# Optimization experiments

Hardware: AMD Instinct MI355X
Metric: run time of the kernel (lower is better)

The kernel has to match this reference:

```python
import jax, jax.numpy as jnp
import numpy as np

B = 1024
NIF = 2048   # n_image_features
V = 10000    # vocab_size
E = 512      # embedding_dim
H = 1024     # hidden_size
L = 32       # max_sentence_length
ND = 3       # num distractors


def _lstm_cell(x, h, c, Wih, Whh, bih, bhh):
    # torch LSTMCell: gates ordered i, f, g, o
    g = x @ Wih.T + bih + h @ Whh.T + bhh
    i, f, gc, o = jnp.split(g, 4, axis=-1)
    c = jax.nn.sigmoid(f) * c + jax.nn.sigmoid(i) * jnp.tanh(gc)
    h = jax.nn.sigmoid(o) * jnp.tanh(c)
    return h, c


def setup_inputs() -> dict:
    key = jax.random.key(0)
    ks = jax.random.split(key, 20)
    s = 0.02
    inp = {
        "target": jax.random.normal(ks[0], (B, NIF), jnp.float32),
        "distractors": jax.random.normal(ks[1], (ND, B, NIF), jnp.float32),
        "start_token_idx": 1,
        "max_sentence_length": L,
        # Sender params
        "W_aff": s * jax.random.normal(ks[2], (H, NIF), jnp.float32),
        "b_aff": jnp.zeros((H,), jnp.float32),
        "emb_s": s * jax.random.normal(ks[3], (V, E), jnp.float32),
        "Wih_s": s * jax.random.normal(ks[4], (4 * H, E), jnp.float32),
        "Whh_s": s * jax.random.normal(ks[5], (4 * H, H), jnp.float32),
        "bih_s": jnp.zeros((4 * H,), jnp.float32),
        "bhh_s": jnp.zeros((4 * H,), jnp.float32),
        "Wp": s * jax.random.normal(ks[6], (V, H), jnp.float32),
        "bp": jnp.zeros((V,), jnp.float32),
        # Receiver params
        "emb_r": s * jax.random.normal(ks[7], (V, E), jnp.float32),
        "Wih_r": s * jax.random.normal(ks[8], (4 * H, E), jnp.float32),
        "Whh_r": s * jax.random.normal(ks[9], (4 * H, H), jnp.float32),
        "bih_r": jnp.zeros((4 * H,), jnp.float32),
        "bhh_r": jnp.zeros((4 * H,), jnp.float32),
        "W_out": s * jax.random.normal(ks[10], (NIF, H), jnp.float32),
        "b_out": jnp.zeros((NIF,), jnp.float32),
    }
    return inp


def reference(target, distractors, start_token_idx, max_sentence_length,
              W_aff, b_aff, emb_s, Wih_s, Whh_s, bih_s, bhh_s, Wp, bp,
              emb_r, Wih_r, Whh_r, bih_r, bhh_r, W_out, b_out):
    Bt = target.shape[0]

    # ---- Sender: greedy decode (eval-mode argmax, matching greedy=True) ----
    h0 = target @ W_aff.T + b_aff
    c0 = jnp.zeros_like(h0)
    w0 = emb_s[jnp.full((Bt,), start_token_idx, dtype=jnp.int32)]

    def send_step(carry, _):
        h, c, w = carry
        h, c = _lstm_cell(w, h, c, Wih_s, Whh_s, bih_s, bhh_s)
        logits = h @ Wp.T + bp                         # [B, V]
        idx = jnp.argmax(logits, axis=-1)              # greedy token
        logp = jnp.take_along_axis(jax.nn.log_softmax(logits, axis=-1),
                                   idx[:, None], axis=-1)[:, 0]
        w = emb_s[idx]
        return (h, c, w), (idx, logp)

    _, (message, logps) = jax.lax.scan(send_step, (h0, c0, w0), None,
                                       length=max_sentence_length)
    message = message.T            # [B, L]
    log_prob = logps[-1]           # log_prob of last sampled word, [B]

    # ---- Receiver: encode message ----
    hr = jnp.zeros((Bt, H), jnp.float32)
    cr = jnp.zeros((Bt, H), jnp.float32)

    def recv_step(carry, w_idx):
        h, c = carry
        h, c = _lstm_cell(emb_r[w_idx], h, c, Wih_r, Whh_r, bih_r, bhh_r)
        return (h, c), None

    (hr, cr), _ = jax.lax.scan(recv_step, (hr, cr), message.T)
    r = hr @ W_out.T + b_out       # [B, NIF]

    # ---- Hinge loss over distractors ----
    r_T = r.T                                       # [NIF, B]
    t_r = target @ r_T                              # [B, B]
    d_r = jnp.einsum('nbf,fc->nbc', distractors, r_T)  # [ND, B, B]
    loss = jnp.sum(jnp.maximum(0.0, 1.0 - t_r[None] + d_r), axis=0)  # [B, B]
    loss = -loss * log_prob        # broadcast [B] over last dim, as in torch
    return jnp.mean(loss)
```

## Files before the change

### kernel.cpp

```cpp
#include <hip/hip_runtime.h>
#include <hip/hip_bf16.h>
#include <cstdint>
#include <cstddef>

#define Bc   1024
#define NIFc 2048
#define Vc   10000
#define Ec   512
#define Hc   1024
#define Lc   32
#define NDc  3
#define G4c  4096
#define NTv  79
#define TMLD 80
#define XLD  3584
#define XOFF 512
#define RLD  1536

typedef __attribute__((ext_vector_type(4))) float f32x4;
typedef __attribute__((ext_vector_type(8))) short s16x8;
typedef __attribute__((ext_vector_type(4))) short s16x4;

__device__ __host__ __forceinline__ int rperm_orig(int p) {
    return ((p >> 4) & 3) * Hc + (p >> 6) * 16 + (p & 15);
// ... 207 lines not shown

    for (int kt = 0; kt < Hc / GBK; ++kt) {
        __syncthreads();
        #pragma unroll
        for (int r = 0; r < 4; ++r) {
            int ldsbase = (r * 256 + wave * 64) * 8;
            gld_lds16(As + ldsbase, ag[r]);
            gld_lds16(Ws + ldsbase, wg[r]);
            ag[r] += GBK;
            wg[r] += GBK;
        }
        __syncthreads();
        #pragma unroll
        for (int c = 0; c < 2; ++c) {
            s16x8 af[4], wf[4];
            int q = c * 4 + quad;
            #pragma unroll
            for (int i = 0; i < 4; ++i) {
                int m = hm + i * 16 + lm;
                af[i] = *(const s16x8*)(As + ((m << 3) + (q ^ (m & 7))) * 8);
                int n = hn + i * 16 + lm;
                wf[i] = *(const s16x8*)(Ws + ((n << 3) + (q ^ (n & 7))) * 8);
            }
            #pragma unroll
            for (int i = 0; i < 4; ++i)
                #pragma unroll
                for (int j = 0; j < 4; ++j)
                    acc[i][j] = __builtin_amdgcn_mfma_f32_16x16x32_bf16(
                        af[i], wf[j], acc[i][j], 0, 0, 0);
        }
    }

    const int u = ((n0 + hn) >> 6) * 16 + lm;
    int pc[4];
    float bv[4];
    #pragma unroll
    for (int g = 0; g < 4; ++g) {
        pc[g] = n0 + hn + g * 16 + lm;
        bv[g] = biasp[pc[g]];
    }
    #pragma unroll
    for (int i = 0; i < 4; ++i) {
        #pragma unroll
        for (int rr = 0; rr < 4; ++rr) {
            int b = m0 + hm + i * 16 + quad * 4 + rr;
            const __hip_bfloat16* xr = Xg + (size_t)tok[b] * G4c;
            float gi = acc[i][0][rr] + bv[0] + __bfloat162float(xr[pc[0]]);
            float gf = acc[i][1][rr] + bv[1] + __bfloat162float(xr[pc[1]]);
            float gg = acc[i][2][rr] + bv[2] + __bfloat162float(xr[pc[2]]);
            float go = acc[i][3][rr] + bv[3] + __bfloat162float(xr[pc[3]]);
            float si = 1.0f / (1.0f + expf(-gi));
            float sf = 1.0f / (1.0f + expf(-gf));
            float so = 1.0f / (1.0f + expf(-go));
            size_t cix = (size_t)b * Hc + u;
            float cc = sf * cr[cix] + si * tanhf(gg);
            cr[cix] = cc;
            xh_out[(size_t)b * RLD + Ec + u] = __float2bfloat16(so * tanhf(cc));
        }
    }
}

__global__ __launch_bounds__(256) void gemm_recv_final(
    const __hip_bfloat16* __restrict__ A, const __hip_bfloat16* __restrict__ W,
    const float* __restrict__ biasp, const __hip_bfloat16* __restrict__ Xg,
    const int* __restrict__ tok, float* __restrict__ cr,
    __hip_bfloat16* __restrict__ xh_out)
{
    __shared__ GemmSmem sm;
    recv_gemm_cell_body(sm, A, W, biasp, Xg, tok, cr, xh_out,
                        blockIdx.x & 31, blockIdx.x >> 5);
}

__global__ __launch_bounds__(256) void gemm_bf16_tn(
    const __hip_bfloat16* __restrict__ A, int lda,
    const __hip_bfloat16* __restrict__ W, int ldw,
    const float* __restrict__ bias, float* __restrict__ C,
    int M, int N, int K, float* __restrict__ tile_max, int tmld)
{
    __shared__ GemmSmem sm;
    gemm_body<0>(sm, A, lda, W, ldw, bias, C, M, N, K, blockIdx.x, blockIdx.y,
                 tile_max, tmld);
}

__global__ __launch_bounds__(256) void gemm_bf16_obf(
    const __hip_bfloat16* __restrict__ A, int lda,
    const __hip_bfloat16* __restrict__ W, int ldw,
    __hip_bfloat16* __restrict__ C, int M, int N, int K)
{
    __shared__ GemmSmem sm;
    gemm_body<1>(sm, A, lda, W, ldw, nullptr, C, M, N, K, blockIdx.x,
                 blockIdx.y, nullptr, 0);
}

__global__ __launch_bounds__(256) void gemm_bf16_sk2(
    const __hip_bfloat16* __restrict__ A, int lda,
    const __hip_bfloat16* __restrict__ W, int ldw,
    float* __restrict__ Cpart, int M, int N, int Ksub)
{
    __shared__ GemmSmem sm;
    int z = blockIdx.z;
    gemm_body<0>(sm, A + (size_t)z * Ksub, lda, W + (size_t)z * Ksub, ldw,
                 nullptr, Cpart + (size_t)z * M * N, M, N, Ksub, blockIdx.x,
                 blockIdx.y, nullptr, 0);
}

template<int LOGBF>
__global__ __launch_bounds__(256) void gemm_fused_step(
    int nb_g,
    const __hip_bfloat16* __restrict__ Ag, const __hip_bfloat16* __restrict__ Wg,
    float* __restrict__ Cg,
    const __hip_bfloat16* __restrict__ Al, const __hip_bfloat16* __restrict__ Wl,
    const float* __restrict__ bl, void* __restrict__ Cl,
    float* __restrict__ tmax,
    const __hip_bfloat16* __restrict__ Ar, const __hip_bfloat16* __restrict__ Wr,
    const float* __restrict__ biasrp, const __hip_bfloat16* __restrict__ Xgr,
    const int* __restrict__ tokr, float* __restrict__ cr,
    __hip_bfloat16* __restrict__ xh_out)
{
    __shared__ GemmSmem sm;
    int bid = blockIdx.x;
    if (bid < nb_g) {
        gemm_body<0>(sm, Ag, XLD, Wg, XLD, nullptr, Cg,
                     Bc, G4c, 3072, bid & 31, bid >> 5, nullptr, 0);
    } else if (bid < nb_g + 632) {
        int rem = bid - nb_g;
        int by = rem / NTv, bx = rem - by * NTv;
        gemm_body<LOGBF>(sm, Al, XLD, Wl, Hc, bl, Cl, Bc, Vc, Hc, bx, by,
                         tmax, TMLD);
    } else {
        int rem = bid - nb_g - 632;
        recv_gemm_cell_body(sm, Ar, Wr, biasrp, Xgr, tokr, cr, xh_out,
                            rem & 31, rem >> 5);
    }
}

__global__ __launch_bounds__(256) void split3_a_kernel(
    const float* __restrict__ in, int ldin,
    __hip_bfloat16* __restrict__ out, int ldo, int coff, int M, int K)
{
    int i = blockIdx.x * 256 + threadIdx.x;
    if (i >= M * K) return;
    int m = i / K, k = i - m * K;
    float v = in[(size_t)m * ldin + k];
    __hip_bfloat16 hi = __float2bfloat16(v);
    float lo = v - __bfloat162float(hi);
    __hip_bfloat16* row = out + (size_t)m * ldo + coff;
    row[k] = hi;
    row[K + k] = __float2bfloat16(lo);
    row[2 * K + k] = hi;
}

__global__ __launch_bounds__(256) void split3_w_kernel(
    const float* __restrict__ in, int ldin,
    __hip_bfloat16* __restrict__ out, int ldo, int coff, int M, int K)
{
    int i = blockIdx.x * 256 + threadIdx.x;
    if (i >= M * K) return;
    int m = i / K, k = i - m * K;
    float v = in[(size_t)m * ldin + k];
    __hip_bfloat16 hi = __float2bfloat16(v);
    float lo = v - __bfloat162float(hi);
    __hip_bfloat16* row = out + (size_t)m * ldo + coff;
    row[k] = hi;
    row[K + k] = hi;
    row[2 * K + k] = __float2bfloat16(lo);
}

__global__ __launch_bounds__(256) void cast2d_kernel(
    const float* __restrict__ in, int ldin,
    __hip_bfloat16* __restrict__ out, int ldo, int coff, int M, int K)
{
    int i = blockIdx.x * 256 + threadIdx.x;
    if (i >= M * K) return;
    int m = i / K, k = i - m * K;
    out[(size_t)m * ldo + coff + k] = __float2bfloat16(in[(size_t)m * ldin + k]);
}

__global__ __launch_bounds__(256) void cast2d_perm_kernel(
    const float* __restrict__ in, int ldin,
    __hip_bfloat16* __restrict__ out, int ldo, int coff, int M, int K)
{
    int i = blockIdx.x * 256 + threadIdx.x;
    if (i >= M * K) return;
    int p = i / K, k = i - p * K;
    out[(size_t)p * ldo + coff + k] =
        __float2bfloat16(in[(size_t)rperm_orig(p) * ldin + k]);
}

__global__ __launch_bounds__(256) void gather_cast_kernel(
    const float* __restrict__ emb, int E, const int* __restrict__ idx,
    int stride, __hip_bfloat16* __restrict__ out, int ldo, int coff, int Brows)
{
    int i = blockIdx.x * 256 + threadIdx.x;
    if (i >= Brows * E) return;
    int b = i / E, k = i - b * E;
    out[(size_t)b * ldo + coff + k] =
        __float2bfloat16(emb[(size_t)idx[(size_t)b * stride] * E + k]);
}

__global__ __launch_bounds__(256) void add_vec_kernel(
    const float* __restrict__ a, const float* __restrict__ b,
    float* __restrict__ o, int n)
{
    int i = blockIdx.x * 256 + threadIdx.x;
    if (i < n) o[i] = a[i] + b[i];
}

__global__ __launch_bounds__(256) void add_vec_perm_kernel(
    const float* __restrict__ a, const float* __restrict__ b,
    float* __restrict__ o, int n)
{
    int i = blockIdx.x * 256 + threadIdx.x;
    if (i < n) { int s = rperm_orig(i); o[i] = a[s] + b[s]; }
}

__device__ __forceinline__ short bf16bits(float x) {
    __hip_bfloat16 t = __float2bfloat16(x);
    return *reinterpret_cast<short*>(&t);
}

__device__ __forceinline__ float b16f(short s) {
    return __bfloat162float(*reinterpret_cast<__hip_bfloat16*>(&s));
}

__global__ __launch_bounds__(256) void lstm_fused_s(
    const float* __restrict__ gp0, const float* __restrict__ gp1,
    const float* __restrict__ bias, float* __restrict__ h,
    float* __restrict__ c, __hip_bfloat16* __restrict__ h3x,
    const __hip_bfloat16* __restrict__ xg, const int* __restrict__ tok,
    int tstride)
{
    int i = blockIdx.x * 256 + threadIdx.x;
    if (i >= Bc * Hc / 4) return;
    int b = i >> 8;
    int j = (i & 255) * 4;
    size_t g0 = (size_t)b * G4c + j;
    f32x4 gi = *(const f32x4*)(gp0 + g0) + *(const f32x4*)(gp1 + g0)
             + *(const f32x4*)(bias + j);
    f32x4 gf = *(const f32x4*)(gp0 + g0 + Hc) + *(const f32x4*)(gp1 + g0 + Hc)
             + *(const f32x4*)(bias + Hc + j);
    f32x4 gg = *(const f32x4*)(gp0 + g0 + 2 * Hc) + *(const f32x4*)(gp1 + g0 + 2 * Hc)
             + *(const f32x4*)(bias + 2 * Hc + j);
    f32x4 go = *(const f32x4*)(gp0 + g0 + 3 * Hc) + *(const f32x4*)(gp1 + g0 + 3 * Hc)
             + *(const f32x4*)(bias + 3 * Hc + j);
    if (xg) {
        const __hip_bfloat16* xr = xg + (size_t)tok[(size_t)b * tstride] * G4c;
        s16x4 xi = *(const s16x4*)(xr + j);
        s16x4 xf = *(const s16x4*)(xr + Hc + j);
        s16x4 xc = *(const s16x4*)(xr + 2 * Hc + j);
        s16x4 xo = *(const s16x4*)(xr + 3 * Hc + j);
        #pragma unroll
        for (int k = 0; k < 4; ++k) {
            gi[k] += b16f(xi[k]);
            gf[k] += b16f(xf[k]);
            gg[k] += b16f(xc[k]);
            go[k] += b16f(xo[k]);
        }
    }
    size_t hix = (size_t)b * Hc + j;
    f32x4 cv = *(const f32x4*)(c + hix);
    f32x4 cn, hv;
    s16x4 hi4, lo4;
    #pragma unroll
    for (int k = 0; k < 4; ++k) {
        float si = 1.0f / (1.0f + expf(-gi[k]));
        float sf = 1.0f / (1.0f + expf(-gf[k]));
        float so = 1.0f / (1.0f + expf(-go[k]));
        float cc = sf * cv[k] + si * tanhf(gg[k]);
        cn[k] = cc;
        float hh = so * tanhf(cc);
        hv[k] = hh;
        hi4[k] = bf16bits(hh);
        lo4[k] = bf16bits(hh - __bfloat162float(__float2bfloat16(hh)));
    }
    *(f32x4*)(c + hix) = cn;
    *(f32x4*)(h + hix) = hv;
    __hip_bfloat16* row = h3x + (size_t)b * XLD + XOFF;
    *(s16x4*)(row + j) = hi4;
    *(s16x4*)(row + Hc + j) = lo4;
    *(s16x4*)(row + 2 * Hc + j) = hi4;
}

__global__ __launch_bounds__(256) void combine_h0_kernel(
    const float* __restrict__ p0, const float* __restrict__ p1,
    const float* __restrict__ bias, float* __restrict__ h,
    __hip_bfloat16* __restrict__ h3x)
{
    int i = blockIdx.x * 256 + threadIdx.x;
    if (i >= Bc * Hc / 4) return;
    int b = i >> 8;
    int j = (i & 255) * 4;
    size_t ix = (size_t)b * Hc + j;
    f32x4 v = *(const f32x4*)(p0 + ix) + *(const f32x4*)(p1 + ix)
            + *(const f32x4*)(bias + j);
    *(f32x4*)(h + ix) = v;
    s16x4 hi4, lo4;
// ... 121 lines not shown
    __syncthreads();
    int nqt = nq < 32 ? nq : 32;

    for (int qi = 0; qi < nqt; qi += 2) {
        int ti = qi + (tid >> 7);
        if (ti < nqt) {
            int j = qt[ti] * 128 + (tid & 127);
            if (j < Vc) {
                float v = row[j];
                if (v >= m - delta) {
                    int k = atomicAdd(&cnt, 1);
                    if (k < 64) cand[k] = j;
                }
            }
        }
    }
    __syncthreads();
    int nc = cnt < 64 ? cnt : 64;

    const float* hrow = h + (size_t)b * Hc;
    for (int cix = wave; cix < nc; cix += 4) {
        int j = cand[cix];
        const float* wrow = Wp + (size_t)j * Hc;
        float part = 0.0f;
        #pragma unroll
        for (int kk = 0; kk < 4; ++kk) {
            int k = kk * 256 + lane * 4;
            f32x4 hv = *(const f32x4*)(hrow + k);
            f32x4 wv = *(const f32x4*)(wrow + k);
            part = fmaf(hv.x, wv.x, part);
            part = fmaf(hv.y, wv.y, part);
            part = fmaf(hv.z, wv.z, part);
            part = fmaf(hv.w, wv.w, part);
        }
        #pragma unroll
        for (int off = 1; off < 64; off <<= 1)
            part += __shfl_xor(part, off);
        if (lane == 0) score[cix] = part + bp[j];
    }
    __syncthreads();
    if (tid == 0) {
        float bv = -__builtin_inff();
        int bj = 0x7fffffff;
        for (int cix = 0; cix < nc; ++cix) {
            float v = score[cix];
            int j = cand[cix];
            if (v > bv || (v == bv && j < bj)) { bv = v; bj = j; }
        }
        sbestv = bv;
        sbestj = bj;
        msg_t[b] = bj;
    }
    __syncthreads();
    const int bestj = sbestj;

    if (want_logp) {
        float s = 0.0f;
        const f32x4* row4 = (const f32x4*)row;
        for (int j = tid; j < Vc / 4; j += 256) {
            f32x4 v = row4[j];
            s += expf(v.x - m) + expf(v.y - m) + expf(v.z - m) + expf(v.w - m);
        }
        redm[tid] = s;
        __syncthreads();
        #pragma unroll
        for (int st = 128; st > 0; st >>= 1) {
            if (tid < st) redm[tid] += redm[tid + st];
            __syncthreads();
        }
        if (tid == 0) logp[b] = sbestv - (m + logf(redm[0]));
    }

    if (xdst && tid < 128) {
        int k = tid * 4;
        f32x4 e = *(const f32x4*)(emb + (size_t)bestj * Ec + k);
        s16x4 h4;
        #pragma unroll
        for (int kk = 0; kk < 4; ++kk) h4[kk] = bf16bits(e[kk]);
        *(s16x4*)(xdst + (size_t)b * XLD + k) = h4;
    }
}

template<int LGBF>
__global__ __launch_bounds__(256) void argmax_lstm_step(
    const void* __restrict__ logits_v, const float* __restrict__ tmax,
    const float* __restrict__ h, const float* __restrict__ Wp,
    const float* __restrict__ bp, int* __restrict__ msg_t,
    float* __restrict__ logp, int want_logp,
    int do_s, const float* __restrict__ gp0,
    const float* __restrict__ bias_s, float* __restrict__ h_s,
    float* __restrict__ c_s, __hip_bfloat16* __restrict__ h3x,
    const __hip_bfloat16* __restrict__ Xg_s)
{
    const int b = blockIdx.x;
    const int tid = threadIdx.x;
    const int lane = tid & 63;
    const int wave = tid >> 6;
    const __hip_bfloat16* rowb = (const __hip_bfloat16*)logits_v + (size_t)b * Vc;
    const float* rowf = (const float*)logits_v + (size_t)b * Vc;

    __shared__ float stm[128];
    __shared__ float redm[256];
    __shared__ float reds[256];
    __shared__ int   qt[32];
    __shared__ int   nq, cnt;
    __shared__ int   cand[64];
    __shared__ float score[64];
    __shared__ float sbestv;
    __shared__ int   sbestj;

    float tv = (tid < NTv) ? tmax[(size_t)b * TMLD + tid] : -__builtin_inff();
    if (tid < 128) stm[tid] = tv;
    redm[tid] = tv;
    reds[tid] = (tid < NTv) ? tv : 0.0f;
    if (tid == 0) { nq = 0; cnt = 0; }
    __syncthreads();
    #pragma unroll
    for (int s = 128; s > 0; s >>= 1) {
        if (tid < s) {
            redm[tid] = fmaxf(redm[tid], redm[tid + s]);
            reds[tid] += reds[tid + s];
        }
        __syncthreads();
    }
    const float m = redm[0];
    const float spread = m - reds[0] * (1.0f / NTv);
    const float delta = 0.08f * spread + 1e-6f * (1.0f + fabsf(m));

    if (tid < NTv && stm[tid] >= m - delta) {
        int k = atomicAdd(&nq, 1);
        if (k < 32) qt[k] = tid;
    }
    __syncthreads();
    int nqt = nq < 32 ? nq : 32;

    for (int qi = 0; qi < nqt; qi += 2) {
        int ti = qi + (tid >> 7);
        if (ti < nqt) {
            int j = qt[ti] * 128 + (tid & 127);
            if (j < Vc) {
                float v = LGBF ? __bfloat162float(rowb[j]) : rowf[j];
                if (v >= m - delta) {
                    int k = atomicAdd(&cnt, 1);
                    if (k < 64) cand[k] = j;
                }
            }
        }
    }
    __syncthreads();
    int nc = cnt < 64 ? cnt : 64;

    const float* hrow = h + (size_t)b * Hc;
    for (int cix = wave; cix < nc; cix += 4) {
        int j = cand[cix];
        const float* wrow = Wp + (size_t)j * Hc;
        float part = 0.0f;
        #pragma unroll
        for (int kk = 0; kk < 4; ++kk) {
            int k = kk * 256 + lane * 4;
            f32x4 hv = *(const f32x4*)(hrow + k);
            f32x4 wv = *(const f32x4*)(wrow + k);
            part = fmaf(hv.x, wv.x, part);
            part = fmaf(hv.y, wv.y, part);
            part = fmaf(hv.z, wv.z, part);
            part = fmaf(hv.w, wv.w, part);
        }
        #pragma unroll
        for (int off = 1; off < 64; off <<= 1)
            part += __shfl_xor(part, off);
        if (lane == 0) score[cix] = part + bp[j];
    }
    __syncthreads();
    if (tid == 0) {
        float bv = -__builtin_inff();
        int bj = 0x7fffffff;
        for (int cix = 0; cix < nc; ++cix) {
            float v = score[cix];
            int j = cand[cix];
            if (v > bv || (v == bv && j < bj)) { bv = v; bj = j; }
        }
        sbestv = bv;
        sbestj = bj;
        msg_t[b] = bj;
    }
    __syncthreads();
    const int tok = sbestj;

    if (!LGBF && want_logp) {
        float s = 0.0f;
        const f32x4* row4 = (const f32x4*)rowf;
        for (int j = tid; j < Vc / 4; j += 256) {
            f32x4 v = row4[j];
// ... 74 lines not shown
        __syncthreads();
    }
    if (tid == 0) partials[blockIdx.x] = sv[0];
}

__global__ __launch_bounds__(256) void final_reduce_kernel(
    const float* __restrict__ partials, int np, float* __restrict__ out,
    float scale)
{
    int tid = threadIdx.x;
    float acc = 0.0f;
    for (int i = tid; i < np; i += 256) acc += partials[i];
    __shared__ float sv[256];
    sv[tid] = acc;
    __syncthreads();
    for (int s = 128; s > 0; s >>= 1) {
        if (tid < s) sv[tid] += sv[tid + s];
        __syncthreads();
    }
    if (tid == 0) out[0] = sv[0] * scale;
}

extern "C" void kernel_launch(void* const* d_in, const int* in_sizes, int n_in,
                              void* d_out, int out_size, void* d_ws, size_t ws_size,
                              hipStream_t stream)
{
    (void)in_sizes; (void)n_in; (void)out_size;

    const float* target  = (const float*)d_in[0];
    const float* distr   = (const float*)d_in[1];
    const int*   start_t = (const int*)d_in[2];
    const float* W_aff = (const float*)d_in[4];
    const float* b_aff = (const float*)d_in[5];
    const float* emb_s = (const float*)d_in[6];
    const float* Wih_s = (const float*)d_in[7];
    const float* Whh_s = (const float*)d_in[8];
    const float* bih_s = (const float*)d_in[9];
    const float* bhh_s = (const float*)d_in[10];
    const float* Wp    = (const float*)d_in[11];
    const float* bp    = (const float*)d_in[12];
    const float* emb_r = (const float*)d_in[13];
    const float* Wih_r = (const float*)d_in[14];
    const float* Whh_r = (const float*)d_in[15];
    const float* bih_r = (const float*)d_in[16];
    const float* bhh_r = (const float*)d_in[17];
    const float* W_out = (const float*)d_in[18];
    const float* b_out = (const float*)d_in[19];

    dim3 blk(256);

    char* b0 = (char*)d_ws;
    size_t off = 0;
    auto take = [&](size_t bytes) -> char* {
        char* p = b0 + off;
        off += (bytes + 511) & ~(size_t)511;
        return p;
    };
    const size_t MB = 1024 * 1024;
    __hip_bfloat16* W3x     = (__hip_bfloat16*)take((size_t)G4c * XLD * 2);
    __hip_bfloat16* Wp_b    = (__hip_bfloat16*)take((size_t)Vc * Hc * 2);
    __hip_bfloat16* WihWhh_r= (__hip_bfloat16*)take((size_t)G4c * RLD * 2);
    __hip_bfloat16* W_out_b = (__hip_bfloat16*)take((size_t)NIFc * Hc * 2);
    __hip_bfloat16* h3x     = (__hip_bfloat16*)take((size_t)Bc * XLD * 2);
    __hip_bfloat16* xh_rA   = (__hip_bfloat16*)take((size_t)Bc * RLD * 2);
    __hip_bfloat16* xh_rB   = (__hip_bfloat16*)take((size_t)Bc * RLD * 2);
    float* gates_p = (float*)take((size_t)2 * Bc * G4c * 4);
    float* h_s    = (float*)take((size_t)Bc * Hc * 4);
    float* c_s    = (float*)take((size_t)Bc * Hc * 4);
    float* hr     = (float*)take((size_t)Bc * Hc * 4);
    float* cr     = (float*)take((size_t)Bc * Hc * 4);
    float* logp   = (float*)take(Bc * 4);
    int*   msg    = (int*)take((size_t)Lc * Bc * 4);
    float* parts  = (float*)take(1024 * 4);
    float* bias_s = (float*)take(G4c * 4);
    float* bias_r = (float*)take(G4c * 4);
    float* tilemax= (float*)take((size_t)Bc * TMLD * 4);
    char*  U      = take(48 * MB);

    __hip_bfloat16* Xg_s = (__hip_bfloat16*)take((size_t)Vc * G4c * 2);
    const int use_tab_s = (off <= ws_size);
    __hip_bfloat16* Xg_r = (__hip_bfloat16*)take((size_t)Vc * G4c * 2);
    const int use_tab_r = (off <= ws_size);
    const int use_merged = use_tab_s && use_tab_r;

    __hip_bfloat16* target3 = (__hip_bfloat16*)U;
    __hip_bfloat16* W_aff3  = (__hip_bfloat16*)(U + 13 * MB);
    __hip_bfloat16* emb_b   = (__hip_bfloat16*)(U + 26 * MB);
    float*          logits  = (float*)U;
    __hip_bfloat16* A4b     = (__hip_bfloat16*)U;
    float*          r_f     = (float*)(U + 17 * MB);
    __hip_bfloat16* r_b     = (__hip_bfloat16*)(U + 26 * MB);
    float*          S       = (float*)(U + 31 * MB);

    cast2d_kernel<<<(G4c * Ec + 255) / 256, blk, 0, stream>>>(
        Wih_s, Ec, W3x, XLD, 0, G4c, Ec);
    split3_w_kernel<<<(G4c * Hc + 255) / 256, blk, 0, stream>>>(
        Whh_s, Hc, W3x, XLD, XOFF, G4c, Hc);
    cast2d_kernel<<<(Vc * Hc + 255) / 256, blk, 0, stream>>>(
        Wp, Hc, Wp_b, Hc, 0, Vc, Hc);
    split3_a_kernel<<<(Bc * NIFc + 255) / 256, blk, 0, stream>>>(
        target, NIFc, target3, 6144, 0, Bc, NIFc);
    split3_w_kernel<<<(Hc * NIFc + 255) / 256, blk, 0, stream>>>(
        W_aff, NIFc, W_aff3, 6144, 0, Hc, NIFc);
    cast2d_perm_kernel<<<(G4c * Ec + 255) / 256, blk, 0, stream>>>(
        Wih_r, Ec, WihWhh_r, RLD, 0, G4c, Ec);
    cast2d_perm_kernel<<<(G4c * Hc + 255) / 256, blk, 0, stream>>>(
        Whh_r, Hc, WihWhh_r, RLD, Ec, G4c, Hc);
    cast2d_kernel<<<(NIFc * Hc + 255) / 256, blk, 0, stream>>>(
        W_out, Hc, W_out_b, Hc, 0, NIFc, Hc);
    add_vec_kernel<<<(G4c + 255) / 256, blk, 0, stream>>>(bih_s, bhh_s,
                                                          bias_s, G4c);
    add_vec_perm_kernel<<<(G4c + 255) / 256, blk, 0, stream>>>(bih_r, bhh_r,
                                                               bias_r, G4c);

    if (use_tab_s) {
        cast2d_kernel<<<(Vc * Ec + 255) / 256, blk, 0, stream>>>(
            emb_s, Ec, emb_b, Ec, 0, Vc, Ec);
        gemm_bf16_obf<<<dim3(G4c / GBN, (Vc + GBM - 1) / GBM), blk, 0, stream>>>(
            emb_b, Ec, W3x, XLD, Xg_s, Vc, G4c, Ec);
    }
    if (use_tab_r) {
        cast2d_kernel<<<(Vc * Ec + 255) / 256, blk, 0, stream>>>(
            emb_r, Ec, emb_b, Ec, 0, Vc, Ec);
        gemm_bf16_obf<<<dim3(G4c / GBN, (Vc + GBM - 1) / GBM), blk, 0, stream>>>(
            emb_b, Ec, WihWhh_r, RLD, Xg_r, Vc, G4c, Ec);
    }

    gemm_bf16_sk2<<<dim3(Hc / GBN, Bc / GBM, 2), blk, 0, stream>>>(
        target3, 6144, W_aff3, 6144, gates_p, Bc, Hc, 3072);
    combine_h0_kernel<<<(Bc * Hc / 4 + 255) / 256, blk, 0, stream>>>(
        gates_p, gates_p + (size_t)Bc * Hc, b_aff, h_s, h3x);
    hipMemsetAsync(c_s, 0, (size_t)Bc * Hc * 4, stream);

    if (use_merged) {
        hipMemsetAsync(cr, 0, (size_t)Bc * Hc * 4, stream);
        hipMemsetAsync(xh_rA, 0, (size_t)Bc * RLD * 2, stream);

        gemm_bf16_sk2<<<dim3(G4c / GBN, Bc / GBM, 2), blk, 0, stream>>>(
            h3x + XOFF, XLD, W3x + XOFF, XLD, gates_p, Bc, G4c, 1536);
        lstm_fused_s<<<(Bc * Hc / 4 + 255) / 256, blk, 0, stream>>>(
            gates_p, gates_p + (size_t)Bc * G4c, bias_s, h_s, c_s, h3x,
            Xg_s, start_t, 0);

        for (int t = 0; t < Lc; ++t) {
            const int do_g = (t < Lc - 1);
            const int do_r = (t >= 1);
            const int k = t - 1;
            const __hip_bfloat16* rin = (k & 1) ? xh_rB : xh_rA;
            __hip_bfloat16* rout = (k & 1) ? xh_rA : xh_rB;
            const int nb = do_g * 256 + 632 + do_r * 256;
            if (t < Lc - 1) {
                gemm_fused_step<1><<<nb, blk, 0, stream>>>(
                    do_g ? 256 : 0,
                    h3x + XOFF, W3x + XOFF, gates_p,
                    h3x + XOFF, Wp_b, bp, (void*)logits, tilemax,
                    do_r ? rin + Ec : nullptr, WihWhh_r + Ec, bias_r, Xg_r,
                    do_r ? msg + (t - 1) * Bc : nullptr, cr, rout);
                argmax_lstm_step<1><<<Bc, blk, 0, stream>>>(
                    (const void*)logits, tilemax, h_s, Wp, bp, msg + t * Bc,
                    logp, 0, 1, gates_p, bias_s, h_s, c_s, h3x, Xg_s);
            } else {
                gemm_fused_step<0><<<nb, blk, 0, stream>>>(
                    0,
                    h3x + XOFF, W3x + XOFF, gates_p,
                    h3x + XOFF, Wp_b, bp, (void*)logits, tilemax,
                    rin + Ec, WihWhh_r + Ec, bias_r, Xg_r,
                    msg + (t - 1) * Bc, cr, rout);
                argmax_lstm_step<0><<<Bc, blk, 0, stream>>>(
                    (const void*)logits, tilemax, h_s, Wp, bp, msg + t * Bc,
                    logp, 1, 0, gates_p, bias_s, h_s, c_s, h3x, Xg_s);
            }
        }
        gemm_recv_final<<<256, blk, 0, stream>>>(
            xh_rB + Ec, WihWhh_r + Ec, bias_r, Xg_r, msg + (Lc - 1) * Bc,
            cr, xh_rA);
    } else {
        if (!use_tab_s)
            gather_cast_kernel<<<(Bc * Ec + 255) / 256, blk, 0, stream>>>(
                emb_s, Ec, start_t, 0, h3x, XLD, 0, Bc);

        for (int t = 0; t < Lc; ++t) {
            if (use_tab_s) {
                gemm_bf16_sk2<<<dim3(G4c / GBN, Bc / GBM, 2), blk, 0, stream>>>(
                    h3x + XOFF, XLD, W3x + XOFF, XLD, gates_p, Bc, G4c, 1536);
                lstm_fused_s<<<(Bc * Hc / 4 + 255) / 256, blk, 0, stream>>>(
                    gates_p, gates_p + (size_t)Bc * G4c, bias_s, h_s, c_s, h3x,
                    Xg_s, (t == 0) ? start_t : (msg + (t - 1) * Bc),
                    (t == 0) ? 0 : 1);
            } else {
                gemm_bf16_sk2<<<dim3(G4c / GBN, Bc / GBM, 2), blk, 0, stream>>>(
                    h3x, XLD, W3x, XLD, gates_p, Bc, G4c, 1792);
                lstm_fused_s<<<(Bc * Hc / 4 + 255) / 256, blk, 0, stream>>>(
                    gates_p, gates_p + (size_t)Bc * G4c, bias_s, h_s, c_s, h3x,
                    nullptr, nullptr, 0);
            }
            gemm_bf16_tn<<<dim3((Vc + GBN - 1) / GBN, Bc / GBM), blk, 0, stream>>>(
                h3x + XOFF, XLD, Wp_b, Hc, bp, logits, Bc, Vc, Hc, tilemax, TMLD);
            argmax_rescore_v3<<<Bc, blk, 0, stream>>>(
                logits, tilemax, h_s, Wp, bp, emb_s, msg + t * Bc, logp,
                (!use_tab_s && t < Lc - 1) ? h3x : nullptr,
                (t == Lc - 1) ? 1 : 0);
        }

        hipMemsetAsync(hr, 0, (size_t)Bc * Hc * 4, stream);
        hipMemsetAsync(cr, 0, (size_t)Bc * Hc * 4, stream);
        hipMemsetAsync(xh_rA, 0, (size_t)Bc * RLD * 2, stream);
        if (!use_tab_r)
            gather_cast_kernel<<<(Bc * Ec + 255) / 256, blk, 0, stream>>>(
                emb_r, Ec, msg, 1, xh_rA, RLD, 0, Bc);
        for (int t = 0; t < Lc; ++t) {
            if (use_tab_r) {
                if (t > 0)
                    gemm_bf16_sk2<<<dim3(G4c / GBN, Bc / GBM, 2), blk, 0, stream>>>(
                        xh_rA + Ec, RLD, WihWhh_r + Ec, RLD, gates_p, Bc, G4c, 512);
                lstm_fused_r<<<(Bc * Hc / 4 + 255) / 256, blk, 0, stream>>>(
                    gates_p, gates_p + (size_t)Bc * G4c, bias_r, hr, cr, xh_rA,
                    Xg_r, msg + t * Bc, (t > 0) ? 1 : 0, nullptr, nullptr);
            } else {
                gemm_bf16_sk2<<<dim3(G4c / GBN, Bc / GBM, 2), blk, 0, stream>>>(
                    xh_rA, RLD, WihWhh_r, RLD, gates_p, Bc, G4c, 768);
                lstm_fused_r<<<(Bc * Hc / 4 + 255) / 256, blk, 0, stream>>>(
                    gates_p, gates_p + (size_t)Bc * G4c, bias_r, hr, cr, xh_rA,
                    nullptr, nullptr, 1, emb_r,
                    (t < Lc - 1) ? (msg + (t + 1) * Bc) : nullptr);
            }
        }
    }

    gemm_bf16_tn<<<dim3(NIFc / GBN, Bc / GBM), blk, 0, stream>>>(
        xh_rA + Ec, RLD, W_out_b, Hc, b_out, r_f, Bc, NIFc, Hc, nullptr, 0);

    cast2d_kernel<<<(Bc * NIFc + 255) / 256, blk, 0, stream>>>(
        target, NIFc, A4b, NIFc, 0, Bc, NIFc);
    cast2d_kernel<<<(NDc * Bc * NIFc + 255) / 256, blk, 0, stream>>>(
        distr, NIFc, A4b + (size_t)Bc * NIFc, NIFc, 0, NDc * Bc, NIFc);
    cast2d_kernel<<<(Bc * NIFc + 255) / 256, blk, 0, stream>>>(
        r_f, NIFc, r_b, NIFc, 0, Bc, NIFc);
    gemm_bf16_tn<<<dim3(Bc / GBN, 4 * Bc / GBM), blk, 0, stream>>>(
        A4b, NIFc, r_b, NIFc, nullptr, S, 4 * Bc, Bc, NIFc, nullptr, 0);

    hinge_kernel<<<1024, blk, 0, stream>>>(S, logp, parts, Bc);
    final_reduce_kernel<<<1, blk, 0, stream>>>(
        parts, 1024, (float*)d_out, -1.0f / ((float)Bc * (float)Bc));
}
```

Measured before the change: 4.504 ms.

## Merge prep casts into one kernel, fuse table GEMMs, move receiver cell into argmax step

```diff
diff --git a/kernel.cpp b/kernel.cpp
--- a/kernel.cpp
+++ b/kernel.cpp
@@ -313,16 +313,6 @@
                  tile_max, tmld);
 }
 
-__global__ __launch_bounds__(256) void gemm_bf16_obf(
-    const __hip_bfloat16* __restrict__ A, int lda,
-    const __hip_bfloat16* __restrict__ W, int ldw,
-    __hip_bfloat16* __restrict__ C, int M, int N, int K)
-{
-    __shared__ GemmSmem sm;
-    gemm_body<1>(sm, A, lda, W, ldw, nullptr, C, M, N, K, blockIdx.x,
-                 blockIdx.y, nullptr, 0);
-}
-
 __global__ __launch_bounds__(256) void gemm_bf16_sk2(
     const __hip_bfloat16* __restrict__ A, int lda,
     const __hip_bfloat16* __restrict__ W, int ldw,
@@ -333,6 +323,33 @@
     gemm_body<0>(sm, A + (size_t)z * Ksub, lda, W + (size_t)z * Ksub, ldw,
                  nullptr, Cpart + (size_t)z * M * N, M, N, Ksub, blockIdx.x,
                  blockIdx.y, nullptr, 0);
+}
+
+__global__ __launch_bounds__(256) void gemm_tab_h0(
+    int nbS, int nbR,
+    const __hip_bfloat16* __restrict__ embS, const __hip_bfloat16* __restrict__ embR,
+    const __hip_bfloat16* __restrict__ W3x, const __hip_bfloat16* __restrict__ Wr,
+    __hip_bfloat16* __restrict__ XgS, __hip_bfloat16* __restrict__ XgR,
+    const __hip_bfloat16* __restrict__ target3,
+    const __hip_bfloat16* __restrict__ W_aff3, float* __restrict__ gates_p)
+{
+    __shared__ GemmSmem sm;
+    int bid = blockIdx.x;
+    if (bid < nbS) {
+        gemm_body<1>(sm, embS, Ec, W3x, XLD, nullptr, XgS,
+                     Vc, G4c, Ec, bid & 31, bid >> 5, nullptr, 0);
+    } else if (bid < nbS + nbR) {
+        int rem = bid - nbS;
+        gemm_body<1>(sm, embR, Ec, Wr, RLD, nullptr, XgR,
+                     Vc, G4c, Ec, rem & 31, rem >> 5, nullptr, 0);
+    } else {
+        int r2 = bid - nbS - nbR;
+        int z = r2 >> 6, rem = r2 & 63;
+        gemm_body<0>(sm, target3 + (size_t)z * 3072, 6144,
+                     W_aff3 + (size_t)z * 3072, 6144, nullptr,
+                     gates_p + (size_t)z * Bc * Hc,
+                     Bc, Hc, 3072, rem & 7, rem >> 3, nullptr, 0);
+    }
 }
 
 template<int LOGBF>
@@ -342,59 +359,109 @@
     float* __restrict__ Cg,
     const __hip_bfloat16* __restrict__ Al, const __hip_bfloat16* __restrict__ Wl,
     const float* __restrict__ bl, void* __restrict__ Cl,
-    float* __restrict__ tmax,
-    const __hip_bfloat16* __restrict__ Ar, const __hip_bfloat16* __restrict__ Wr,
-    const float* __restrict__ biasrp, const __hip_bfloat16* __restrict__ Xgr,
-    const int* __restrict__ tokr, float* __restrict__ cr,
-    __hip_bfloat16* __restrict__ xh_out)
+    float* __restrict__ tmax)
 {
     __shared__ GemmSmem sm;
     int bid = blockIdx.x;
     if (bid < nb_g) {
         gemm_body<0>(sm, Ag, XLD, Wg, XLD, nullptr, Cg,
                      Bc, G4c, 3072, bid & 31, bid >> 5, nullptr, 0);
-    } else if (bid < nb_g + 632) {
+    } else {
         int rem = bid - nb_g;
         int by = rem / NTv, bx = rem - by * NTv;
         gemm_body<LOGBF>(sm, Al, XLD, Wl, Hc, bl, Cl, Bc, Vc, Hc, bx, by,
                          tmax, TMLD);
-    } else {
-        int rem = bid - nb_g - 632;
-        recv_gemm_cell_body(sm, Ar, Wr, biasrp, Xgr, tokr, cr, xh_out,
-                            rem & 31, rem >> 5);
-    }
-}
-
-__global__ __launch_bounds__(256) void split3_a_kernel(
-    const float* __restrict__ in, int ldin,
-    __hip_bfloat16* __restrict__ out, int ldo, int coff, int M, int K)
+    }
+}
+
+#define PC0  2097152
+#define PC1  6291456
+#define PC2  16531456
+#define PC3  18628608
+#define PC4  20725760
+#define PC5  22822912
+#define PC6  27017216
+#define PC7  29114368
+#define PC8  29118464
+#define PC9  29122560
+#define PC10 34242560
+#define PC11 39362560
+#define PC12 41459712
+#define PC13 47751168
+
+__global__ __launch_bounds__(256) void prep_all_kernel(
+    const float* __restrict__ Wih_s, const float* __restrict__ Whh_s,
+    const float* __restrict__ Wp, const float* __restrict__ target,
+    const float* __restrict__ W_aff, const float* __restrict__ Wih_r,
+    const float* __restrict__ Whh_r, const float* __restrict__ W_out,
+    const float* __restrict__ bih_s, const float* __restrict__ bhh_s,
+    const float* __restrict__ bih_r, const float* __restrict__ bhh_r,
+    const float* __restrict__ emb_s, const float* __restrict__ emb_r,
+    const float* __restrict__ distr,
+    __hip_bfloat16* __restrict__ W3x, __hip_bfloat16* __restrict__ Wp_b,
+    __hip_bfloat16* __restrict__ target3, __hip_bfloat16* __restrict__ W_aff3,
+    __hip_bfloat16* __restrict__ WihWhh_r, __hip_bfloat16* __restrict__ W_out_b,
+    float* __restrict__ bias_s, float* __restrict__ bias_r,
+    __hip_bfloat16* __restrict__ embS, __hip_bfloat16* __restrict__ embR,
+    __hip_bfloat16* __restrict__ A4b)
 {
     int i = blockIdx.x * 256 + threadIdx.x;
-    if (i >= M * K) return;
-    int m = i / K, k = i - m * K;
-    float v = in[(size_t)m * ldin + k];
-    __hip_bfloat16 hi = __float2bfloat16(v);
-    float lo = v - __bfloat162float(hi);
-    __hip_bfloat16* row = out + (size_t)m * ldo + coff;
-    row[k] = hi;
-    row[K + k] = __float2bfloat16(lo);
-    row[2 * K + k] = hi;
-}
-
-__global__ __launch_bounds__(256) void split3_w_kernel(
-    const float* __restrict__ in, int ldin,
-    __hip_bfloat16* __restrict__ out, int ldo, int coff, int M, int K)
-{
-    int i = blockIdx.x * 256 + threadIdx.x;
-    if (i >= M * K) return;
-    int m = i / K, k = i - m * K;
-    float v = in[(size_t)m * ldin + k];
-    __hip_bfloat16 hi = __float2bfloat16(v);
-    float lo = v - __bfloat162float(hi);
-    __hip_bfloat16* row = out + (size_t)m * ldo + coff;
-    row[k] = hi;
-    row[K + k] = hi;
-    row[2 * K + k] = __float2bfloat16(lo);
+    if (i < PC0) {
+        W3x[(size_t)(i / Ec) * XLD + (i % Ec)] = __float2bfloat16(Wih_s[i]);
+    } else if (i < PC1) {
+        int k = i - PC0; int m = k / Hc, c = k - m * Hc;
+        float v = Whh_s[k];
+        __hip_bfloat16 hi = __float2bfloat16(v);
+        float lo = v - __bfloat162float(hi);
+        __hip_bfloat16* row = W3x + (size_t)m * XLD + XOFF;
+        row[c] = hi; row[Hc + c] = hi; row[2 * Hc + c] = __float2bfloat16(lo);
+    } else if (i < PC2) {
+        int k = i - PC1;
+        Wp_b[k] = __float2bfloat16(Wp[k]);
+    } else if (i < PC3) {
+        int k = i - PC2; int m = k / NIFc, c = k - m * NIFc;
+        float v = target[k];
+        __hip_bfloat16 hi = __float2bfloat16(v);
+        float lo = v - __bfloat162float(hi);
+        __hip_bfloat16* row = target3 + (size_t)m * 6144;
+        row[c] = hi; row[NIFc + c] = __float2bfloat16(lo); row[2 * NIFc + c] = hi;
+    } else if (i < PC4) {
+        int k = i - PC3; int m = k / NIFc, c = k - m * NIFc;
+        float v = W_aff[k];
+        __hip_bfloat16 hi = __float2bfloat16(v);
+        float lo = v - __bfloat162float(hi);
+        __hip_bfloat16* row = W_aff3 + (size_t)m * 6144;
+        row[c] = hi; row[NIFc + c] = hi; row[2 * NIFc + c] = __float2bfloat16(lo);
+    } else if (i < PC5) {
+        int k = i - PC4; int p = k / Ec, c = k - p * Ec;
+        WihWhh_r[(size_t)p * RLD + c] =
+            __float2bfloat16(Wih_r[(size_t)rperm_orig(p) * Ec + c]);
+    } else if (i < PC6) {
+        int k = i - PC5; int p = k / Hc, c = k - p * Hc;
+        WihWhh_r[(size_t)p * RLD + Ec + c] =
+            __float2bfloat16(Whh_r[(size_t)rperm_orig(p) * Hc + c]);
+    } else if (i < PC7) {
+        int k = i - PC6;
+        W_out_b[k] = __float2bfloat16(W_out[k]);
+    } else if (i < PC8) {
+        int k = i - PC7;
+        bias_s[k] = bih_s[k] + bhh_s[k];
+    } else if (i < PC9) {
+        int k = i - PC8; int s = rperm_orig(k);
+        bias_r[k] = bih_r[s] + bhh_r[s];
+    } else if (i < PC10) {
+        int k = i - PC9;
+        embS[k] = __float2bfloat16(emb_s[k]);
+    } else if (i < PC11) {
+        int k = i - PC10;
+        embR[k] = __float2bfloat16(emb_r[k]);
+    } else if (i < PC12) {
+        int k = i - PC11;
+        A4b[k] = __float2bfloat16(target[k]);
+    } else if (i < PC13) {
+        int k = i - PC12;
+        A4b[(size_t)Bc * NIFc + k] = __float2bfloat16(distr[k]);
+    }
 }
 
 __global__ __launch_bounds__(256) void cast2d_kernel(
@@ -405,17 +472,6 @@
     if (i >= M * K) return;
     int m = i / K, k = i - m * K;
     out[(size_t)m * ldo + coff + k] = __float2bfloat16(in[(size_t)m * ldin + k]);
-}
-
-__global__ __launch_bounds__(256) void cast2d_perm_kernel(
-    const float* __restrict__ in, int ldin,
-    __hip_bfloat16* __restrict__ out, int ldo, int coff, int M, int K)
-{
-    int i = blockIdx.x * 256 + threadIdx.x;
-    if (i >= M * K) return;
-    int p = i / K, k = i - p * K;
-    out[(size_t)p * ldo + coff + k] =
-        __float2bfloat16(in[(size_t)rperm_orig(p) * ldin + k]);
 }
 
 __global__ __launch_bounds__(256) void gather_cast_kernel(
@@ -427,22 +483,6 @@
     int b = i / E, k = i - b * E;
     out[(size_t)b * ldo + coff + k] =
         __float2bfloat16(emb[(size_t)idx[(size_t)b * stride] * E + k]);
-}
-
-__global__ __launch_bounds__(256) void add_vec_kernel(
-    const float* __restrict__ a, const float* __restrict__ b,
-    float* __restrict__ o, int n)
-{
-    int i = blockIdx.x * 256 + threadIdx.x;
-    if (i < n) o[i] = a[i] + b[i];
-}
-
-__global__ __launch_bounds__(256) void add_vec_perm_kernel(
-    const float* __restrict__ a, const float* __restrict__ b,
-    float* __restrict__ o, int n)
-{
-    int i = blockIdx.x * 256 + threadIdx.x;
-    if (i < n) { int s = rperm_orig(i); o[i] = a[s] + b[s]; }
 }
 
 __device__ __forceinline__ short bf16bits(float x) {
@@ -730,7 +770,12 @@
 }
 
 template<int LGBF>
-__global__ __launch_bounds__(256) void argmax_lstm_step(
+__global__ __launch_bounds__(256) void argmax_cell_recv(
+    int nb_r,
+    const __hip_bfloat16* __restrict__ Ar, const __hip_bfloat16* __restrict__ Wr,
+    const float* __restrict__ biasrp, const __hip_bfloat16* __restrict__ Xgr,
+    const int* __restrict__ tokr, float* __restrict__ cr,
+    __hip_bfloat16* __restrict__ xh_out,
     const void* __restrict__ logits_v, const float* __restrict__ tmax,
     const float* __restrict__ h, const float* __restrict__ Wp,
     const float* __restrict__ bp, int* __restrict__ msg_t,
@@ -740,22 +785,28 @@
     float* __restrict__ c_s, __hip_bfloat16* __restrict__ h3x,
     const __hip_bfloat16* __restrict__ Xg_s)
 {
-    const int b = blockIdx.x;
+    __shared__ GemmSmem sm;
+    __shared__ int nq, cnt, sbestj;
+    __shared__ float sbestv;
+
+    if ((int)blockIdx.x < nb_r) {
+        recv_gemm_cell_body(sm, Ar, Wr, biasrp, Xgr, tokr, cr, xh_out,
+                            blockIdx.x & 31, blockIdx.x >> 5);
+        return;
+    }
+    const int b = blockIdx.x - nb_r;
     const int tid = threadIdx.x;
     const int lane = tid & 63;
     const int wave = tid >> 6;
     const __hip_bfloat16* rowb = (const __hip_bfloat16*)logits_v + (size_t)b * Vc;
     const float* rowf = (const float*)logits_v + (size_t)b * Vc;
 
-    __shared__ float stm[128];
-    __shared__ float redm[256];
-    __shared__ float reds[256];
-    __shared__ int   qt[32];
-    __shared__ int   nq, cnt;
-    __shared__ int   cand[64];
-    __shared__ float score[64];
-    __shared__ float sbestv;
-    __shared__ int   sbestj;
+    float* stm  = (float*)sm.As;
+    float* redm = stm + 128;
+    float* reds = redm + 256;
+    int*   qt   = (int*)(reds + 256);
+    int*   cand = qt + 32;
+    float* score= (float*)(cand + 64);
 
     float tv = (tid < NTv) ? tmax[(size_t)b * TMLD + tid] : -__builtin_inff();
     if (tid < 128) stm[tid] = tv;
@@ -996,52 +1047,37 @@
     __hip_bfloat16* Xg_r = (__hip_bfloat16*)take((size_t)Vc * G4c * 2);
     const int use_tab_r = (off <= ws_size);
     const int use_merged = use_tab_s && use_tab_r;
+    __hip_bfloat16* A4b_ws = (__hip_bfloat16*)take((size_t)4 * Bc * NIFc * 2);
+    __hip_bfloat16* r_b_ws = (__hip_bfloat16*)take((size_t)Bc * NIFc * 2);
+    const int use_extra = (off <= ws_size);
 
     __hip_bfloat16* target3 = (__hip_bfloat16*)U;
     __hip_bfloat16* W_aff3  = (__hip_bfloat16*)(U + 13 * MB);
-    __hip_bfloat16* emb_b   = (__hip_bfloat16*)(U + 26 * MB);
+    __hip_bfloat16* emb_bS  = (__hip_bfloat16*)(U + 26 * MB);
+    __hip_bfloat16* emb_bR  = (__hip_bfloat16*)(U + 36 * MB);
     float*          logits  = (float*)U;
-    __hip_bfloat16* A4b     = (__hip_bfloat16*)U;
+    __hip_bfloat16* A4b_u   = (__hip_bfloat16*)U;
     float*          r_f     = (float*)(U + 17 * MB);
-    __hip_bfloat16* r_b     = (__hip_bfloat16*)(U + 26 * MB);
+    __hip_bfloat16* r_b_u   = (__hip_bfloat16*)(U + 26 * MB);
     float*          S       = (float*)(U + 31 * MB);
 
-    cast2d_kernel<<<(G4c * Ec + 255) / 256, blk, 0, stream>>>(
-        Wih_s, Ec, W3x, XLD, 0, G4c, Ec);
-    split3_w_kernel<<<(G4c * Hc + 255) / 256, blk, 0, stream>>>(
-        Whh_s, Hc, W3x, XLD, XOFF, G4c, Hc);
-    cast2d_kernel<<<(Vc * Hc + 255) / 256, blk, 0, stream>>>(
-        Wp, Hc, Wp_b, Hc, 0, Vc, Hc);
-    split3_a_kernel<<<(Bc * NIFc + 255) / 256, blk, 0, stream>>>(
-        target, NIFc, target3, 6144, 0, Bc, NIFc);
-    split3_w_kernel<<<(Hc * NIFc + 255) / 256, blk, 0, stream>>>(
-        W_aff, NIFc, W_aff3, 6144, 0, Hc, NIFc);
-    cast2d_perm_kernel<<<(G4c * Ec + 255) / 256, blk, 0, stream>>>(
-        Wih_r, Ec, WihWhh_r, RLD, 0, G4c, Ec);
-    cast2d_perm_kernel<<<(G4c * Hc + 255) / 256, blk, 0, stream>>>(
-        Whh_r, Hc, WihWhh_r, RLD, Ec, G4c, Hc);
-    cast2d_kernel<<<(NIFc * Hc + 255) / 256, blk, 0, stream>>>(
-        W_out, Hc, W_out_b, Hc, 0, NIFc, Hc);
-    add_vec_kernel<<<(G4c + 255) / 256, blk, 0, stream>>>(bih_s, bhh_s,
-                                                          bias_s, G4c);
-    add_vec_perm_kernel<<<(G4c + 255) / 256, blk, 0, stream>>>(bih_r, bhh_r,
-                                                               bias_r, G4c);
-
-    if (use_tab_s) {
-        cast2d_kernel<<<(Vc * Ec + 255) / 256, blk, 0, stream>>>(
-            emb_s, Ec, emb_b, Ec, 0, Vc, Ec);
-        gemm_bf16_obf<<<dim3(G4c / GBN, (Vc + GBM - 1) / GBM), blk, 0, stream>>>(
-            emb_b, Ec, W3x, XLD, Xg_s, Vc, G4c, Ec);
-    }
-    if (use_tab_r) {
-        cast2d_kernel<<<(Vc * Ec + 255) / 256, blk, 0, stream>>>(
-            emb_r, Ec, emb_b, Ec, 0, Vc, Ec);
-        gemm_bf16_obf<<<dim3(G4c / GBN, (Vc + GBM - 1) / GBM), blk, 0, stream>>>(
-            emb_b, Ec, WihWhh_r, RLD, Xg_r, Vc, G4c, Ec);
-    }
-
-    gemm_bf16_sk2<<<dim3(Hc / GBN, Bc / GBM, 2), blk, 0, stream>>>(
-        target3, 6144, W_aff3, 6144, gates_p, Bc, Hc, 3072);
+    __hip_bfloat16* A4b = use_extra ? A4b_ws : A4b_u;
+    __hip_bfloat16* r_b = use_extra ? r_b_ws : r_b_u;
+
+    const int base_blocks  = (PC11 + 255) / 256;
+    const int extra_blocks = (PC13 + 255) / 256;
+    prep_all_kernel<<<use_extra ? extra_blocks : base_blocks, blk, 0, stream>>>(
+        Wih_s, Whh_s, Wp, target, W_aff, Wih_r, Whh_r, W_out,
+        bih_s, bhh_s, bih_r, bhh_r, emb_s, emb_r, distr,
+        W3x, Wp_b, target3, W_aff3, WihWhh_r, W_out_b, bias_s, bias_r,
+        emb_bS, emb_bR, A4b);
+
+    const int nbS = use_tab_s ? 2528 : 0;
+    const int nbR = use_tab_r ? 2528 : 0;
+    gemm_tab_h0<<<nbS + nbR + 128, blk, 0, stream>>>(
+        nbS, nbR, emb_bS, emb_bR, W3x, WihWhh_r, Xg_s, Xg_r,
+        target3, W_aff3, gates_p);
+
     combine_h0_kernel<<<(Bc * Hc / 4 + 255) / 256, blk, 0, stream>>>(
         gates_p, gates_p + (size_t)Bc * Hc, b_aff, h_s, h3x);
     hipMemsetAsync(c_s, 0, (size_t)Bc * Hc * 4, stream);
@@ -1058,29 +1094,28 @@
 
         for (int t = 0; t < Lc; ++t) {
             const int do_g = (t < Lc - 1);
-            const int do_r = (t >= 1);
+            const int nb_r = (t >= 1) ? 256 : 0;
             const int k = t - 1;
             const __hip_bfloat16* rin = (k & 1) ? xh_rB : xh_rA;
             __hip_bfloat16* rout = (k & 1) ? xh_rA : xh_rB;
-            const int nb = do_g * 256 + 632 + do_r * 256;
             if (t < Lc - 1) {
-                gemm_fused_step<1><<<nb, blk, 0, stream>>>(
+                gemm_fused_step<1><<<do_g * 256 + 632, blk, 0, stream>>>(
                     do_g ? 256 : 0,
                     h3x + XOFF, W3x + XOFF, gates_p,
-                    h3x + XOFF, Wp_b, bp, (void*)logits, tilemax,
-                    do_r ? rin + Ec : nullptr, WihWhh_r + Ec, bias_r, Xg_r,
-                    do_r ? msg + (t - 1) * Bc : nullptr, cr, rout);
-                argmax_lstm_step<1><<<Bc, blk, 0, stream>>>(
+                    h3x + XOFF, Wp_b, bp, (void*)logits, tilemax);
+                argmax_cell_recv<1><<<nb_r + Bc, blk, 0, stream>>>(
+                    nb_r, rin + Ec, WihWhh_r + Ec, bias_r, Xg_r,
+                    (t >= 1) ? msg + (t - 1) * Bc : msg, cr, rout,
                     (const void*)logits, tilemax, h_s, Wp, bp, msg + t * Bc,
                     logp, 0, 1, gates_p, bias_s, h_s, c_s, h3x, Xg_s);
             } else {
-                gemm_fused_step<0><<<nb, blk, 0, stream>>>(
+                gemm_fused_step<0><<<632, blk, 0, stream>>>(
                     0,
                     h3x + XOFF, W3x + XOFF, gates_p,
-                    h3x + XOFF, Wp_b, bp, (void*)logits, tilemax,
-                    rin + Ec, WihWhh_r + Ec, bias_r, Xg_r,
-                    msg + (t - 1) * Bc, cr, rout);
-                argmax_lstm_step<0><<<Bc, blk, 0, stream>>>(
+                    h3x + XOFF, Wp_b, bp, (void*)logits, tilemax);
+                argmax_cell_recv<0><<<nb_r + Bc, blk, 0, stream>>>(
+                    nb_r, rin + Ec, WihWhh_r + Ec, bias_r, Xg_r,
+                    msg + (t - 1) * Bc, cr, rout,
                     (const void*)logits, tilemax, h_s, Wp, bp, msg + t * Bc,
                     logp, 1, 0, gates_p, bias_s, h_s, c_s, h3x, Xg_s);
             }
@@ -1144,10 +1179,12 @@
     gemm_bf16_tn<<<dim3(NIFc / GBN, Bc / GBM), blk, 0, stream>>>(
         xh_rA + Ec, RLD, W_out_b, Hc, b_out, r_f, Bc, NIFc, Hc, nullptr, 0);
 
-    cast2d_kernel<<<(Bc * NIFc + 255) / 256, blk, 0, stream>>>(
-        target, NIFc, A4b, NIFc, 0, Bc, NIFc);
-    cast2d_kernel<<<(NDc * Bc * NIFc + 255) / 256, blk, 0, stream>>>(
-        distr, NIFc, A4b + (size_t)Bc * NIFc, NIFc, 0, NDc * Bc, NIFc);
+    if (!use_extra) {
+        cast2d_kernel<<<(Bc * NIFc + 255) / 256, blk, 0, stream>>>(
+            target, NIFc, A4b, NIFc, 0, Bc, NIFc);
+        cast2d_kernel<<<(NDc * Bc * NIFc + 255) / 256, blk, 0, stream>>>(
+            distr, NIFc, A4b + (size_t)Bc * NIFc, NIFc, 0, NDc * Bc, NIFc);
+    }
     cast2d_kernel<<<(Bc * NIFc + 255) / 256, blk, 0, stream>>>(
         r_f, NIFc, r_b, NIFc, 0, Bc, NIFc);
     gemm_bf16_tn<<<dim3(Bc / GBN, 4 * Bc / GBM), blk, 0, stream>>>(
```

Result: no change. 4.486 ms (-0.4%).
